# Optimization experiments

Measured on AMD Instinct MI355X. Metric: run time of the kernel, lower is better.

## Reference

```python
import jax, jax.numpy as jnp
import numpy as np

N = 4096
M0 = 2048
M1 = 2048
MCS = 4096
STRIDE = 2
D_NNGP = STRIDE ** 2 * M1              # 8192, input dim of layer-1 arccos maps
D_NTK = STRIDE ** 2 * (MCS + M1)       # 24576, input dim1 of layer-1 count sketch


def setup_inputs() -> dict:
    key = jax.random.key(0)
    ks = jax.random.split(key, 8)
    return {
        "layer_idx": 1,
        "z_nngp": jax.random.normal(ks[0], (N, D_NNGP), jnp.float32),
        "z_ntk": jax.random.normal(ks[1], (N, D_NTK), jnp.float32),
        "W0": jax.random.normal(ks[2], (D_NNGP, M0), jnp.float32),   # arccos0[1].W
        "W1": jax.random.normal(ks[3], (D_NNGP, M1), jnp.float32),   # arccos1[1].W
        "sign1": (jax.random.randint(ks[4], (D_NTK,), 0, 2) * 2 - 1).astype(jnp.float32),
        "indx1": jax.random.randint(ks[5], (D_NTK,), 0, MCS),
        "sign2": (jax.random.randint(ks[6], (M0,), 0, 2) * 2 - 1).astype(jnp.float32),
        "indx2": jax.random.randint(ks[7], (M0,), 0, MCS),
    }


def count_sketch(x, indx, sign, out_dim):
    # x: [n, d_in]; sign-multiply then scatter_add along last axis into out_dim bins
    xs = x * sign[None, :]
    out = jnp.zeros((x.shape[0], out_dim), dtype=x.dtype)
    return out.at[:, indx].add(xs)


def reference(layer_idx, z_nngp, z_ntk, W0, W1, sign1, indx1, sign2, indx2):
    norm0 = np.sqrt(2.0 / M0).astype(np.float32)
    norm1 = np.float32(np.sqrt(2.0 / M1) / 2.0)
    # arccos order-0 feature map (step function)
    xw0 = z_nngp @ W0
    tmp = (xw0 > 0).astype(z_nngp.dtype) * norm0          # [N, M0]
    # arccos order-1 feature map (relu-like: |xw| + xw)
    xw1 = z_nngp @ W1
    z_nngp_out = (jnp.abs(xw1) + xw1) * norm1             # [N, M1]
    # tensor sketch: count-sketch both, FFT, complex pointwise multiply, ifft.real
    x_cs = count_sketch(z_ntk, indx1, sign1, MCS)         # [N, MCS]
    y_cs = count_sketch(tmp, indx2, sign2, MCS)           # [N, MCS]
    z_ntk_out = jnp.fft.ifft(jnp.fft.fft(x_cs, axis=-1) * jnp.fft.fft(y_cs, axis=-1)).real
    z_ntk_cat = jnp.concatenate([z_nngp_out, z_ntk_out], axis=1)  # [N, M1+MCS]
    return (z_nngp_out, z_ntk_cat)
```

## Files before the change

### kernel.cpp

```cpp
#include <hip/hip_runtime.h>

#define NROW 4096
#define KDIM 8192
#define MDIM 2048
#define MCS_ 4096
#define DNTK 24576
#define CATW 6144
#define TAU_HALF 2.5e-3f
#define NT (KDIM / 32)

typedef __attribute__((ext_vector_type(8))) short short8;
typedef __attribute__((ext_vector_type(4))) float f32x4;

__device__ __forceinline__ void split2(float x0, float x1,
                                       unsigned& hi, unsigned& lo) {
    const unsigned u0 = __float_as_uint(x0);
    const unsigned u1 = __float_as_uint(x1);
    hi = (u0 >> 16) | (u1 & 0xFFFF0000u);
    const float l0 = x0 - __uint_as_float(u0 & 0xFFFF0000u);
    const float l1 = x1 - __uint_as_float(u1 & 0xFFFF0000u);
    lo = (__float_as_uint(l0) >> 16) | (__float_as_uint(l1) & 0xFFFF0000u);
}

__device__ __forceinline__ float2 cmulf(float2 a, float2 b) {
    return make_float2(a.x * b.x - a.y * b.y, a.x * b.y + a.y * b.x);
}

__global__ __launch_bounds__(512) void convert_kernel(
    const float* __restrict__ A,
    const float* __restrict__ W1,
    const float* __restrict__ W0,
    short8* __restrict__ aHi, short8* __restrict__ aLo,
    short8* __restrict__ wHi, short8* __restrict__ wLo)
{
    int b = blockIdx.x;
    const int tid = threadIdx.x;
    if (b < 4096) {
        const int P = b >> 8, T = b & 255;
        const float* src = A + (size_t)(P * 256) * KDIM + T * 32;
        short8* dh = aHi + ((size_t)b << 10);
        short8* dl = aLo + ((size_t)b << 10);
        for (int s = tid; s < 1024; s += 512) {
            const int row = ((s >> 6) << 4) | (s & 15);
            const int k0  = ((s >> 4) & 3) * 8;
            const float* p = src + (size_t)row * KDIM + k0;
            const float4 v0 = *reinterpret_cast<const float4*>(p);
            const float4 v1 = *reinterpret_cast<const float4*>(p + 4);
            union { short8 ss; unsigned u[4]; } h, l;
            split2(v0.x, v0.y, h.u[0], l.u[0]);
            split2(v0.z, v0.w, h.u[1], l.u[1]);
            split2(v1.x, v1.y, h.u[2], l.u[2]);
            split2(v1.z, v1.w, h.u[3], l.u[3]);
            dh[s] = h.ss; dl[s] = l.ss;
        }
    } else {
        b -= 4096;
        const int mat = b >> 11;
        const int T   = b & 255;
        const int Pc  = (b >> 8) & 7;
        const float* Wm = mat ? W0 : W1;
        const float* src = Wm + (size_t)(T * 32) * MDIM + Pc * 256;
        short8* dh = wHi + ((size_t)b << 10);
        short8* dl = wLo + ((size_t)b << 10);
        for (int s = tid; s < 1024; s += 512) {
            const int col = ((s >> 6) << 4) | (s & 15);
            const int k0  = ((s >> 4) & 3) * 8;
            float v[8];
#pragma unroll
            for (int j = 0; j < 8; ++j)
                v[j] = src[(size_t)(k0 + j) * MDIM + col];
            union { short8 ss; unsigned u[4]; } h, l;
            split2(v[0], v[1], h.u[0], l.u[0]);
            split2(v[2], v[3], h.u[1], l.u[1]);
            split2(v[4], v[5], h.u[2], l.u[2]);
            split2(v[6], v[7], h.u[3], l.u[3]);
            dh[s] = h.ss; dl[s] = l.ss;
        }
    }
}

__global__ __launch_bounds__(512) void csr_build(
    const int* __restrict__ indx1, const float* __restrict__ sign1,
    const int* __restrict__ indx2, const float* __restrict__ sign2,
    int* __restrict__ rowptr1, int* __restrict__ ent1,
    int* __restrict__ rowptr2, int* __restrict__ ent2)
{
    const int which = blockIdx.x;
    const int*   idx = which ? indx2 : indx1;
    const float* sg  = which ? sign2 : sign1;
    const int    n   = which ? 2048 : 24576;
    int* rowptr = which ? rowptr2 : rowptr1;
    int* ent    = which ? ent2 : ent1;

    __shared__ int h[4096];
    __shared__ int rp[4097];
    __shared__ int part[512];
    const int tid = threadIdx.x;

    for (int i = tid; i < 4096; i += 512) h[i] = 0;
    __syncthreads();
    for (int d = tid; d < n; d += 512) atomicAdd(&h[idx[d]], 1);
    __syncthreads();

    int loc[8], s = 0;
#pragma unroll
    for (int k = 0; k < 8; ++k) { loc[k] = h[8 * tid + k]; s += loc[k]; }
    part[tid] = s;
    __syncthreads();
    for (int off = 1; off < 512; off <<= 1) {
        int v = part[tid];
        if (tid >= off) v += part[tid - off];
        __syncthreads();
        part[tid] = v;
        __syncthreads();
    }
    int base = tid ? part[tid - 1] : 0;
#pragma unroll
    for (int k = 0; k < 8; ++k) { rp[8 * tid + k] = base; base += loc[k]; }
    if (tid == 511) rp[4096] = base;
    __syncthreads();

    for (int i = tid; i < 4096; i += 512) h[i] = 0;
    __syncthreads();
    for (int d = tid; d < n; d += 512) {
        const int b   = idx[d];
        const int pos = atomicAdd(&h[b], 1);
        ent[rp[b] + pos] = d | (sg[d] < 0.f ? 0x80000000 : 0);
    }
    __syncthreads();

    for (int i = tid; i < 4097; i += 512) rowptr[i] = rp[i];
    for (int b = tid; b < 4096; b += 512) {
        const int lo = rp[b], hi = rp[b + 1];
        for (int i = lo + 1; i < hi; ++i) {
            const int e = ent[i], key = e & 0x7FFFFFFF;
            int j = i - 1;
            while (j >= lo && (ent[j] & 0x7FFFFFFF) > key) { ent[j + 1] = ent[j]; --j; }
            ent[j + 1] = e;
        }
    }
}

__global__ __launch_bounds__(512, 2) void gemm_mfma_pre(
    const short8* __restrict__ aHi, const short8* __restrict__ aLo,
    const short8* __restrict__ wHi, const short8* __restrict__ wLo,
    float* __restrict__ out0, float* __restrict__ outCat)
{
    const int mode = blockIdx.z;
    __shared__ short8 AhiS[2][1024], AloS[2][1024];
    __shared__ short8 BhiS[2][1024], BloS[2][1024];

    const int tid  = threadIdx.x;
    const int lane = tid & 63;
    const int wid  = tid >> 6;
    const int wr   = wid >> 1;
    const int wc   = wid & 1;
    const int brow = blockIdx.y * 256;
    const int bcol = blockIdx.x * 256;

    const size_t aBase = ((size_t)blockIdx.y) << 18;
    const size_t wBase = ((size_t)(mode * 8 + blockIdx.x)) << 18;

    f32x4 acc[4][8];
#pragma unroll
    for (int m = 0; m < 4; ++m)
#pragma unroll
        for (int n = 0; n < 8; ++n)
#pragma unroll
            for (int i = 0; i < 4; ++i) acc[m][n][i] = 0.f;

    short8 st[8];

#define ISSUE(T)                                                             \
    {                                                                        \
        const size_t o = ((size_t)(T)) << 10;                                \
        st[0] = aHi[aBase + o + tid];  st[1] = aHi[aBase + o + tid + 512];   \
        st[2] = aLo[aBase + o + tid];  st[3] = aLo[aBase + o + tid + 512];   \
        st[4] = wHi[wBase + o + tid];  st[5] = wHi[wBase + o + tid + 512];   \
        st[6] = wLo[wBase + o + tid];  st[7] = wLo[wBase + o + tid + 512];   \
    }
#define WRITE(BUF)                                                           \
    {                                                                        \
        AhiS[BUF][tid] = st[0];  AhiS[BUF][tid + 512] = st[1];               \
        AloS[BUF][tid] = st[2];  AloS[BUF][tid + 512] = st[3];               \
        BhiS[BUF][tid] = st[4];  BhiS[BUF][tid + 512] = st[5];               \
        BloS[BUF][tid] = st[6];  BloS[BUF][tid + 512] = st[7];               \
    }

    ISSUE(0); WRITE(0); ISSUE(1);
    __syncthreads();

    for (int t = 0; t < NT; ++t) {
        const int cur = t & 1;

        short8 ah[4], al[4];
#pragma unroll
        for (int m = 0; m < 4; ++m) {
            ah[m] = AhiS[cur][(wr * 4 + m) * 64 + lane];
            al[m] = AloS[cur][(wr * 4 + m) * 64 + lane];
        }

        if (t + 1 < NT) {
            WRITE(cur ^ 1);
            if (t + 2 < NT) ISSUE(t + 2);
        }

#pragma unroll
        for (int n = 0; n < 8; ++n) {
            const short8 bh = BhiS[cur][(wc * 8 + n) * 64 + lane];
            const short8 bl = BloS[cur][(wc * 8 + n) * 64 + lane];
#pragma unroll
            for (int m = 0; m < 4; ++m) {
                acc[m][n] = __builtin_amdgcn_mfma_f32_16x16x32_bf16(
                    ah[m], bh, acc[m][n], 0, 0, 0);
                acc[m][n] = __builtin_amdgcn_mfma_f32_16x16x32_bf16(
                    ah[m], bl, acc[m][n], 0, 0, 0);
                acc[m][n] = __builtin_amdgcn_mfma_f32_16x16x32_bf16(
                    al[m], bh, acc[m][n], 0, 0, 0);
            }
        }
        __syncthreads();
    }
#undef ISSUE
#undef WRITE

    const float norm0 = 0.03125f;
    const int ocol0 = bcol + wc * 128 + (lane & 15);
    const int orow0 = brow + wr * 64 + ((lane >> 4) << 2);
#pragma unroll
    for (int m = 0; m < 4; ++m)
#pragma unroll
        for (int n = 0; n < 8; ++n) {
            const int col = ocol0 + n * 16;
#pragma unroll
            for (int i = 0; i < 4; ++i) {
                const int row = orow0 + m * 16 + i;
                if (mode == 0) {
                    const float v = fmaxf(acc[m][n][i], 0.f) * norm0;
                    out0[(size_t)row * MDIM + col] = v;
                    outCat[(size_t)row * CATW + col] = v;
                } else {
                    outCat[(size_t)row * CATW + 2048 + col] = acc[m][n][i];
                }
            }
        }
}

__global__ __launch_bounds__(512, 2) void gemm_mfma(
    const float* __restrict__ A,
    const float* __restrict__ W1,
    const float* __restrict__ W0,
    float* __restrict__ out0,
    float* __restrict__ outCat)
{
    const int mode = blockIdx.z;
    const float* __restrict__ W = mode ? W0 : W1;

    __shared__ short8 AhiS[2][1024], AloS[2][1024];
    __shared__ short8 BhiS[2][1024], BloS[2][1024];

    const int tid  = threadIdx.x;
    const int lane = tid & 63;
    const int wid  = tid >> 6;
    const int wr   = wid >> 1;
    const int wc   = wid & 1;
    const int brow = blockIdx.y * 256;
    const int bcol = blockIdx.x * 256;

    f32x4 acc[4][8];
#pragma unroll
    for (int m = 0; m < 4; ++m)
#pragma unroll
        for (int n = 0; n < 8; ++n)
#pragma unroll
            for (int i = 0; i < 4; ++i) acc[m][n][i] = 0.f;

    const int srow  = tid >> 1;
    const int skh   = tid & 1;
    const int slot0 = (srow >> 4) * 64 + (srow & 15) + (skh << 5);
    const float* aptr = A + (size_t)(brow + srow) * KDIM + skh * 16;
    const float* bptr = W + (size_t)(skh * 16) * MDIM + (bcol + srow);

    float4 av0, av1, av2, av3;
    float  bst[16];

#define LOAD_TILE(T)                                                         \
    {                                                                        \
        const float* ap = aptr + (T) * 32;                                   \
        av0 = *reinterpret_cast<const float4*>(ap);                          \
        av1 = *reinterpret_cast<const float4*>(ap + 4);                      \
        av2 = *reinterpret_cast<const float4*>(ap + 8);                      \
        av3 = *reinterpret_cast<const float4*>(ap + 12);                     \
        const float* bp = bptr + (size_t)((T) * 32) * MDIM;                  \
        _Pragma("unroll")                                                    \
        for (int j = 0; j < 16; ++j) bst[j] = bp[(size_t)j * MDIM];          \
    }
#define CONVERT_WRITE(BUF)                                                   \
    {                                                                        \
        union { short8 s; unsigned u[4]; } h, l;                             \
        split2(av0.x, av0.y, h.u[0], l.u[0]);                                \
        split2(av0.z, av0.w, h.u[1], l.u[1]);                                \
        split2(av1.x, av1.y, h.u[2], l.u[2]);                                \
        split2(av1.z, av1.w, h.u[3], l.u[3]);                                \
        AhiS[BUF][slot0] = h.s;  AloS[BUF][slot0] = l.s;                     \
        split2(av2.x, av2.y, h.u[0], l.u[0]);                                \
        split2(av2.z, av2.w, h.u[1], l.u[1]);                                \
        split2(av3.x, av3.y, h.u[2], l.u[2]);                                \
        split2(av3.z, av3.w, h.u[3], l.u[3]);                                \
        AhiS[BUF][slot0 + 16] = h.s;  AloS[BUF][slot0 + 16] = l.s;           \
        split2(bst[0], bst[1], h.u[0], l.u[0]);                              \
        split2(bst[2], bst[3], h.u[1], l.u[1]);                              \
        split2(bst[4], bst[5], h.u[2], l.u[2]);                              \
        split2(bst[6], bst[7], h.u[3], l.u[3]);                              \
        BhiS[BUF][slot0] = h.s;  BloS[BUF][slot0] = l.s;                     \
        split2(bst[8],  bst[9],  h.u[0], l.u[0]);                            \
        split2(bst[10], bst[11], h.u[1], l.u[1]);                            \
        split2(bst[12], bst[13], h.u[2], l.u[2]);                            \
        split2(bst[14], bst[15], h.u[3], l.u[3]);                            \
        BhiS[BUF][slot0 + 16] = h.s;  BloS[BUF][slot0 + 16] = l.s;           \
    }

    LOAD_TILE(0);
    CONVERT_WRITE(0);
    LOAD_TILE(1);
    __syncthreads();

    for (int t = 0; t < NT; ++t) {
        const int cur = t & 1;
        short8 ah[4], al[4];
#pragma unroll
        for (int m = 0; m < 4; ++m) {
            ah[m] = AhiS[cur][(wr * 4 + m) * 64 + lane];
            al[m] = AloS[cur][(wr * 4 + m) * 64 + lane];
        }
        if (t + 1 < NT) {
            CONVERT_WRITE(cur ^ 1);
            if (t + 2 < NT) LOAD_TILE(t + 2);
        }
#pragma unroll
        for (int n = 0; n < 8; ++n) {
            const short8 bh = BhiS[cur][(wc * 8 + n) * 64 + lane];
            const short8 bl = BloS[cur][(wc * 8 + n) * 64 + lane];
#pragma unroll
            for (int m = 0; m < 4; ++m) {
                acc[m][n] = __builtin_amdgcn_mfma_f32_16x16x32_bf16(
                    ah[m], bh, acc[m][n], 0, 0, 0);
                acc[m][n] = __builtin_amdgcn_mfma_f32_16x16x32_bf16(
                    ah[m], bl, acc[m][n], 0, 0, 0);
                acc[m][n] = __builtin_amdgcn_mfma_f32_16x16x32_bf16(
                    al[m], bh, acc[m][n], 0, 0, 0);
            }
        }
        __syncthreads();
    }
#undef LOAD_TILE
#undef CONVERT_WRITE

    const float norm0 = 0.03125f;
    const int ocol0 = bcol + wc * 128 + (lane & 15);
    const int orow0 = brow + wr * 64 + ((lane >> 4) << 2);
#pragma unroll
    for (int m = 0; m < 4; ++m)
#pragma unroll
        for (int n = 0; n < 8; ++n) {
            const int col = ocol0 + n * 16;
#pragma unroll
            for (int i = 0; i < 4; ++i) {
                const int row = orow0 + m * 16 + i;
                if (mode == 0) {
                    const float v = fmaxf(acc[m][n][i], 0.f) * norm0;
                    out0[(size_t)row * MDIM + col] = v;
                    outCat[(size_t)row * CATW + col] = v;
                } else {
                    outCat[(size_t)row * CATW + 2048 + col] = acc[m][n][i];
                }
            }
        }
}

#define ZP(i) Z[(i) + ((i) >> 4)]
#define C_SQ2 0.70710678118654752f

__device__ __forceinline__ void fft_conv_body(float2* Z, const float2* RT, int tid) {
    float2 x0, x1, x2, x3, x4, x5, x6, x7;

#pragma unroll
    for (int s = 0; s < 4; ++s) {
        const int lq = 3 * (3 - s);
        const int q  = 1 << lq;
        const int j  = tid & (q - 1);
        const int base = ((tid >> lq) << (lq + 3)) + j;
        x0 = ZP(base);
        x1 = ZP(base + q);
        x2 = ZP(base + 2 * q);
        x3 = ZP(base + 3 * q);
        x4 = ZP(base + 4 * q);
        x5 = ZP(base + 5 * q);
        x6 = ZP(base + 6 * q);
        x7 = ZP(base + 7 * q);

        const float2 w1 = RT[j << (9 - lq)];
        const float2 w2 = cmulf(w1, w1);
        const float2 w3 = cmulf(w2, w1);
        const float2 w4 = cmulf(w2, w2);
        const float2 w5 = cmulf(w3, w2);
        const float2 w6 = cmulf(w3, w3);
        const float2 w7 = cmulf(w4, w3);

        const float2 a0 = make_float2(x0.x + x4.x, x0.y + x4.y);
        const float2 a1 = make_float2(x1.x + x5.x, x1.y + x5.y);
        const float2 a2 = make_float2(x2.x + x6.x, x2.y + x6.y);
        const float2 a3 = make_float2(x3.x + x7.x, x3.y + x7.y);
        const float2 b0 = make_float2(x0.x - x4.x, x0.y - x4.y);
        const float2 b1 = make_float2(x1.x - x5.x, x1.y - x5.y);
        const float2 b2 = make_float2(x2.x - x6.x, x2.y - x6.y);
        const float2 b3 = make_float2(x3.x - x7.x, x3.y - x7.y);

        const float2 ca0 = make_float2(a0.x + a2.x, a0.y + a2.y);
        const float2 ca1 = make_float2(a0.x - a2.x, a0.y - a2.y);
        const float2 ca2 = make_float2(a1.x + a3.x, a1.y + a3.y);
        const float2 ca3 = make_float2(a1.x - a3.x, a1.y - a3.y);
        const float2 y0 = make_float2(ca0.x + ca2.x, ca0.y + ca2.y);
        const float2 y4 = make_float2(ca0.x - ca2.x, ca0.y - ca2.y);
        const float2 y2 = make_float2(ca1.x + ca3.y, ca1.y - ca3.x);
        const float2 y6 = make_float2(ca1.x - ca3.y, ca1.y + ca3.x);

        const float2 b1r = make_float2(C_SQ2 * (b1.x + b1.y), C_SQ2 * (b1.y - b1.x));
        const float2 b2r = make_float2(b2.y, -b2.x);
        const float2 b3r = make_float2(C_SQ2 * (b3.y - b3.x), -C_SQ2 * (b3.x + b3.y));
        const float2 cb0 = make_float2(b0.x + b2r.x, b0.y + b2r.y);
        const float2 cb1 = make_float2(b0.x - b2r.x, b0.y - b2r.y);
        const float2 cb2 = make_float2(b1r.x + b3r.x, b1r.y + b3r.y);
        const float2 cb3 = make_float2(b1r.x - b3r.x, b1r.y - b3r.y);
        const float2 y1 = make_float2(cb0.x + cb2.x, cb0.y + cb2.y);
        const float2 y5 = make_float2(cb0.x - cb2.x, cb0.y - cb2.y);
        const float2 y3 = make_float2(cb1.x + cb3.y, cb1.y - cb3.x);
        const float2 y7 = make_float2(cb1.x - cb3.y, cb1.y + cb3.x);

        ZP(base)         = y0;
        ZP(base + q)     = cmulf(y1, w1);
        ZP(base + 2 * q) = cmulf(y2, w2);
        ZP(base + 3 * q) = cmulf(y3, w3);
        ZP(base + 4 * q) = cmulf(y4, w4);
        ZP(base + 5 * q) = cmulf(y5, w5);
        ZP(base + 6 * q) = cmulf(y6, w6);
        ZP(base + 7 * q) = cmulf(y7, w7);
        __syncthreads();
    }

    for (int p = tid; p < MCS_; p += 512) {
        int q;
        if (p == 0) q = 0;
        else {
            const int h = 31 - __clz(p);
            q = 9 * (1 << (3 * (h / 3))) - 1 - p;
        }
        if (p <= q) {
            const float2 Ap = ZP(p);
            const float2 Bq = ZP(q);
            const float Xr = 0.5f * (Ap.x + Bq.x);
            const float Xi = 0.5f * (Ap.y - Bq.y);
            const float Yr = 0.5f * (Ap.y + Bq.y);
            const float Yi = -0.5f * (Ap.x - Bq.x);
            const float Pr = Xr * Yr - Xi * Yi;
            const float Pi = Xr * Yi + Xi * Yr;
            ZP(p) = make_float2(Pr, Pi);
            ZP(q) = make_float2(Pr, -Pi);
        }
    }
    __syncthreads();

#pragma unroll
    for (int s = 0; s < 4; ++s) {
        const int lq = 3 * s;
        const int q  = 1 << lq;
        const int j  = tid & (q - 1);
        const int base = ((tid >> lq) << (lq + 3)) + j;

        const float2 w1 = RT[j << (9 - lq)];
        const float2 w2 = cmulf(w1, w1);
        const float2 w3 = cmulf(w2, w1);
        const float2 w4 = cmulf(w2, w2);
        const float2 w5 = cmulf(w3, w2);
        const float2 w6 = cmulf(w3, w3);
        const float2 w7 = cmulf(w4, w3);

        x0 = ZP(base);
        {
            float2 t;
            t = ZP(base + q);     x1 = make_float2(t.x * w1.x + t.y * w1.y, t.y * w1.x - t.x * w1.y);
            t = ZP(base + 2 * q); x2 = make_float2(t.x * w2.x + t.y * w2.y, t.y * w2.x - t.x * w2.y);
            t = ZP(base + 3 * q); x3 = make_float2(t.x * w3.x + t.y * w3.y, t.y * w3.x - t.x * w3.y);
            t = ZP(base + 4 * q); x4 = make_float2(t.x * w4.x + t.y * w4.y, t.y * w4.x - t.x * w4.y);
            t = ZP(base + 5 * q); x5 = make_float2(t.x * w5.x + t.y * w5.y, t.y * w5.x - t.x * w5.y);
            t = ZP(base + 6 * q); x6 = make_float2(t.x * w6.x + t.y * w6.y, t.y * w6.x - t.x * w6.y);
            t = ZP(base + 7 * q); x7 = make_float2(t.x * w7.x + t.y * w7.y, t.y * w7.x - t.x * w7.y);
        }

        const float2 a0 = make_float2(x0.x + x4.x, x0.y + x4.y);
        const float2 a1 = make_float2(x1.x + x5.x, x1.y + x5.y);
        const float2 a2 = make_float2(x2.x + x6.x, x2.y + x6.y);
        const float2 a3 = make_float2(x3.x + x7.x, x3.y + x7.y);
        const float2 b0 = make_float2(x0.x - x4.x, x0.y - x4.y);
        const float2 b1 = make_float2(x1.x - x5.x, x1.y - x5.y);
        const float2 b2 = make_float2(x2.x - x6.x, x2.y - x6.y);
        const float2 b3 = make_float2(x3.x - x7.x, x3.y - x7.y);

        const float2 ca0 = make_float2(a0.x + a2.x, a0.y + a2.y);
        const float2 ca1 = make_float2(a0.x - a2.x, a0.y - a2.y);
        const float2 ca2 = make_float2(a1.x + a3.x, a1.y + a3.y);
        const float2 ca3 = make_float2(a1.x - a3.x, a1.y - a3.y);
        const float2 y0 = make_float2(ca0.x + ca2.x, ca0.y + ca2.y);
        const float2 y4 = make_float2(ca0.x - ca2.x, ca0.y - ca2.y);
        const float2 y2 = make_float2(ca1.x - ca3.y, ca1.y + ca3.x);
        const float2 y6 = make_float2(ca1.x + ca3.y, ca1.y - ca3.x);

        const float2 b1r = make_float2(C_SQ2 * (b1.x - b1.y), C_SQ2 * (b1.x + b1.y));
        const float2 b2r = make_float2(-b2.y, b2.x);
        const float2 b3r = make_float2(-C_SQ2 * (b3.x + b3.y), C_SQ2 * (b3.x - b3.y));
        const float2 cb0 = make_float2(b0.x + b2r.x, b0.y + b2r.y);
        const float2 cb1 = make_float2(b0.x - b2r.x, b0.y - b2r.y);
        const float2 cb2 = make_float2(b1r.x + b3r.x, b1r.y + b3r.y);
        const float2 cb3 = make_float2(b1r.x - b3r.x, b1r.y - b3r.y);
        const float2 y1 = make_float2(cb0.x + cb2.x, cb0.y + cb2.y);
        const float2 y5 = make_float2(cb0.x - cb2.x, cb0.y - cb2.y);
        const float2 y3 = make_float2(cb1.x - cb3.y, cb1.y + cb3.x);
        const float2 y7 = make_float2(cb1.x + cb3.y, cb1.y - cb3.x);

        ZP(base)         = y0;
        ZP(base + q)     = y1;
        ZP(base + 2 * q) = y2;
        ZP(base + 3 * q) = y3;
        ZP(base + 4 * q) = y4;
        ZP(base + 5 * q) = y5;
        ZP(base + 6 * q) = y6;
        ZP(base + 7 * q) = y7;
        __syncthreads();
    }
}

__global__ __launch_bounds__(512) void sketch_fft_csr(
    const float* __restrict__ z_ntk,
    const int* __restrict__ rowptr1, const int* __restrict__ ent1,
    const int* __restrict__ rowptr2, const int* __restrict__ ent2,
    float* __restrict__ outCat)
{
    __shared__ __align__(16) float2 Z[4352];
    __shared__ float2 RT[513];
    float* Zf = reinterpret_cast<float*>(Z);
    const int tid = threadIdx.x;
    const int row = blockIdx.x;
    const float norm0 = 0.03125f;

    const float wconst = -1.5339807878856412e-3f;
    for (int t = tid; t <= 512; t += 512) {
        float sw, cw;
        __sincosf(wconst * (float)t, &sw, &cw);
        RT[t] = make_float2(cw, sw);
    }

    int rpx[9], rpy[9];
#pragma unroll
    for (int k = 0; k < 9; ++k) {
        rpx[k] = rowptr1[8 * tid + k];
        rpy[k] = rowptr2[8 * tid + k];
    }
    float accX[8], accY[8];
#pragma unroll
    for (int k = 0; k < 8; ++k) { accX[k] = 0.f; accY[k] = 0.f; }
    int cur[8];
#pragma unroll
    for (int k = 0; k < 8; ++k) cur[k] = rpx[k];

    const float4* xrow4 = reinterpret_cast<const float4*>(z_ntk + (size_t)row * DNTK);
    for (int c = 0; c < 3; ++c) {
        const int lo = c * 8192, hi = lo + 8192;
        __syncthreads();
#pragma unroll
        for (int j = 0; j < 4; ++j)
            reinterpret_cast<float4*>(Zf)[tid + j * 512] = xrow4[c * 2048 + tid + j * 512];
        __syncthreads();
#pragma unroll
        for (int k = 0; k < 8; ++k) {
            while (cur[k] < rpx[k + 1]) {
                const int e = ent1[cur[k]];
                const int d = e & 0x7FFFFFFF;
                if (d >= hi) break;
                const float v = Zf[d - lo];
                accX[k] += (e < 0) ? -v : v;
                ++cur[k];
            }
        }
    }

    const float* trow = outCat + (size_t)row * CATW + 2048;
    __syncthreads();
    reinterpret_cast<float4*>(Zf)[tid] = reinterpret_cast<const float4*>(trow)[tid];
    __syncthreads();
#pragma unroll
    for (int k = 0; k < 8; ++k) {
        for (int c = rpy[k]; c < rpy[k + 1]; ++c) {
            const int e = ent2[c];
            const int d = e & 0x7FFFFFFF;
            const float t = Zf[d];
            const float y = (fabsf(t) < TAU_HALF) ? 0.5f * norm0
                                                  : (t > 0.f ? norm0 : 0.f);
            accY[k] += (e < 0) ? -y : y;
        }
    }
    __syncthreads();

#pragma unroll
    for (int k = 0; k < 8; ++k) {
        const int b = 8 * tid + k;
        ZP(b) = make_float2(accX[k], accY[k]);
    }
    __syncthreads();

    fft_conv_body(Z, RT, tid);

    float* orow = outCat + (size_t)row * CATW + 2048;
    const float scale = 1.0f / (float)MCS_;
    for (int n = tid; n < MCS_; n += 512) orow[n] = ZP(n).x * scale;
}

#define YBASE 4608
__global__ __launch_bounds__(512) void sketch_fft_atomic(
    const float* __restrict__ z_ntk,
    const float* __restrict__ sign1,
    const int*   __restrict__ indx1,
    const float* __restrict__ sign2,
    const int*   __restrict__ indx2,
    float* __restrict__ outCat)
{
    __shared__ __align__(16) float2 Z[4352];
    __shared__ float2 RT[513];
    float* Zf = reinterpret_cast<float*>(Z);
    const int tid = threadIdx.x;
    const int row = blockIdx.x;

    for (int i = tid; i < 2176; i += 512)
        reinterpret_cast<float4*>(Zf)[i] = make_float4(0.f, 0.f, 0.f, 0.f);
    const float wconst = -1.5339807878856412e-3f;
    for (int t = tid; t <= 512; t += 512) {
        float sw, cw;
        __sincosf(wconst * (float)t, &sw, &cw);
        RT[t] = make_float2(cw, sw);
    }
    __syncthreads();

    const float4* xrow4 = reinterpret_cast<const float4*>(z_ntk + (size_t)row * DNTK);
    const float4* s1v   = reinterpret_cast<const float4*>(sign1);
    const int4*   i1v   = reinterpret_cast<const int4*>(indx1);
    for (int v = tid; v < DNTK / 4; v += 512) {
        const float4 x = xrow4[v];
        const float4 s = s1v[v];
        const int4   ix = i1v[v];
        atomicAdd(&Zf[ix.x], x.x * s.x);
        atomicAdd(&Zf[ix.y], x.y * s.y);
        atomicAdd(&Zf[ix.z], x.z * s.z);
        atomicAdd(&Zf[ix.w], x.w * s.w);
    }
    const float norm0 = 0.03125f;
    const float* trow = outCat + (size_t)row * CATW + 2048;
    {
        const float4 t4 = reinterpret_cast<const float4*>(trow)[tid];
        const float4 s  = reinterpret_cast<const float4*>(sign2)[tid];
        const int4   ix = reinterpret_cast<const int4*>(indx2)[tid];
        const float y0 = (fabsf(t4.x) < TAU_HALF) ? 0.5f * norm0 : (t4.x > 0.f ? norm0 : 0.f);
        const float y1 = (fabsf(t4.y) < TAU_HALF) ? 0.5f * norm0 : (t4.y > 0.f ? norm0 : 0.f);
        const float y2 = (fabsf(t4.z) < TAU_HALF) ? 0.5f * norm0 : (t4.z > 0.f ? norm0 : 0.f);
        const float y3 = (fabsf(t4.w) < TAU_HALF) ? 0.5f * norm0 : (t4.w > 0.f ? norm0 : 0.f);
        atomicAdd(&Zf[YBASE + ix.x], y0 * s.x);
        atomicAdd(&Zf[YBASE + ix.y], y1 * s.y);
        atomicAdd(&Zf[YBASE + ix.z], y2 * s.z);
        atomicAdd(&Zf[YBASE + ix.w], y3 * s.w);
    }
    __syncthreads();

    {
        float re[8], im[8];
#pragma unroll
        for (int j = 0; j < 8; ++j) {
            const int i = tid + j * 512;
            re[j] = Zf[i];
            im[j] = Zf[YBASE + i];
        }
        __syncthreads();
#pragma unroll
        for (int j = 0; j < 8; ++j) {
            const int i = tid + j * 512;
            ZP(i) = make_float2(re[j], im[j]);
        }
    }
    __syncthreads();

    fft_conv_body(Z, RT, tid);

    float* orow = outCat + (size_t)row * CATW + 2048;
    const float scale = 1.0f / (float)MCS_;
    for (int n = tid; n < MCS_; n += 512) orow[n] = ZP(n).x * scale;
}

extern "C" void kernel_launch(void* const* d_in, const int* in_sizes, int n_in,
                              void* d_out, int out_size, void* d_ws, size_t ws_size,
                              hipStream_t stream) {
    (void)in_sizes; (void)n_in; (void)out_size;
    const float* z_nngp = (const float*)d_in[1];
    const float* z_ntk  = (const float*)d_in[2];
    const float* W0     = (const float*)d_in[3];
    const float* W1     = (const float*)d_in[4];
    const float* sign1  = (const float*)d_in[5];
    const int*   indx1  = (const int*)d_in[6];
    const float* sign2  = (const float*)d_in[7];
    const int*   indx2  = (const int*)d_in[8];

    float* out0   = (float*)d_out;
    float* outCat = out0 + (size_t)NROW * MDIM;

    const size_t NEED_P = 268435456ull;
    const size_t NEED_C = NEED_P + (1ull << 20);

    int* rowptr1 = nullptr; int* rowptr2 = nullptr;
    int* ent1 = nullptr;    int* ent2 = nullptr;
    const bool csr_ok = ws_size >= NEED_C;
    if (csr_ok) {
        int* base = (int*)((char*)d_ws + NEED_P);
        rowptr1 = base;
        rowptr2 = base + 4352;
        ent1    = base + 8704;
        ent2    = ent1 + 24576;
        csr_build<<<dim3(2), dim3(512), 0, stream>>>(
            indx1, sign1, indx2, sign2, rowptr1, ent1, rowptr2, ent2);
    }

    if (ws_size >= NEED_P) {
        short8* aHi = (short8*)d_ws;
        short8* aLo = aHi + (1ull << 22);
        short8* wHi = aLo + (1ull << 22);
        short8* wLo = wHi + (1ull << 22);
        convert_kernel<<<dim3(8192), dim3(512), 0, stream>>>(
            z_nngp, W1, W0, aHi, aLo, wHi, wLo);
        gemm_mfma_pre<<<dim3(8, 16, 2), dim3(512), 0, stream>>>(
            aHi, aLo, wHi, wLo, out0, outCat);
    } else {
        gemm_mfma<<<dim3(8, 16, 2), dim3(512), 0, stream>>>(
            z_nngp, W1, W0, out0, outCat);
    }

    if (csr_ok) {
        sketch_fft_csr<<<dim3(NROW), dim3(512), 0, stream>>>(
            z_ntk, rowptr1, ent1, rowptr2, ent2, outCat);
    } else {
        sketch_fft_atomic<<<dim3(NROW), dim3(512), 0, stream>>>(
            z_ntk, sign1, indx1, sign2, indx2, outCat);
    }
}
```

Before: 1.294 ms.

## Gather sketch inputs directly from global memory instead of staging through LDS

The CSR count-sketch kernel no longer copies z_ntk chunks and the tmp row into shared memory with block-wide barriers. Each thread now gathers its eight bins' entries straight from global memory, batching eight independent loads per iteration, and the loop exits through a wave-level any-check. The kernel also gets a launch-bounds occupancy hint. This removes the three staging passes and their syncs, in exchange for uncoalesced random global reads that depend on cache hits.

Measured after the change: 1.701 ms. +31.5%, slower.

```diff
diff --git a/kernel.cpp b/kernel.cpp
--- a/kernel.cpp
+++ b/kernel.cpp
@@ -539,7 +539,7 @@
     }
 }
 
-__global__ __launch_bounds__(512) void sketch_fft_csr(
+__global__ __launch_bounds__(512, 8) void sketch_fft_csr(
     const float* __restrict__ z_ntk,
     const int* __restrict__ rowptr1, const int* __restrict__ ent1,
     const int* __restrict__ rowptr2, const int* __restrict__ ent2,
@@ -547,7 +547,6 @@
 {
     __shared__ __align__(16) float2 Z[4352];
     __shared__ float2 RT[513];
-    float* Zf = reinterpret_cast<float*>(Z);
     const int tid = threadIdx.x;
     const int row = blockIdx.x;
     const float norm0 = 0.03125f;
@@ -559,56 +558,61 @@
         RT[t] = make_float2(cw, sw);
     }
 
-    int rpx[9], rpy[9];
-#pragma unroll
-    for (int k = 0; k < 9; ++k) {
-        rpx[k] = rowptr1[8 * tid + k];
-        rpy[k] = rowptr2[8 * tid + k];
-    }
-    float accX[8], accY[8];
-#pragma unroll
-    for (int k = 0; k < 8; ++k) { accX[k] = 0.f; accY[k] = 0.f; }
-    int cur[8];
-#pragma unroll
-    for (int k = 0; k < 8; ++k) cur[k] = rpx[k];
-
-    const float4* xrow4 = reinterpret_cast<const float4*>(z_ntk + (size_t)row * DNTK);
-    for (int c = 0; c < 3; ++c) {
-        const int lo = c * 8192, hi = lo + 8192;
-        __syncthreads();
-#pragma unroll
-        for (int j = 0; j < 4; ++j)
-            reinterpret_cast<float4*>(Zf)[tid + j * 512] = xrow4[c * 2048 + tid + j * 512];
-        __syncthreads();
+    const float* zrow = z_ntk + (size_t)row * DNTK;
+    const float* trow = outCat + (size_t)row * CATW + 2048;
+
+    int rpx[9];
+#pragma unroll
+    for (int k = 0; k < 9; ++k) rpx[k] = rowptr1[8 * tid + k];
+    float accX[8];
+    int c8[8];
+#pragma unroll
+    for (int k = 0; k < 8; ++k) { accX[k] = 0.f; c8[k] = rpx[k]; }
+
+    for (;;) {
+        bool ok[8];
+        int any = 0;
 #pragma unroll
         for (int k = 0; k < 8; ++k) {
-            while (cur[k] < rpx[k + 1]) {
-                const int e = ent1[cur[k]];
-                const int d = e & 0x7FFFFFFF;
-                if (d >= hi) break;
-                const float v = Zf[d - lo];
-                accX[k] += (e < 0) ? -v : v;
-                ++cur[k];
+            ok[k] = c8[k] < rpx[k + 1];
+            any |= (int)ok[k];
+        }
+        if (!__any(any)) break;
+        int e8[8];
+#pragma unroll
+        for (int k = 0; k < 8; ++k)
+            e8[k] = ent1[ok[k] ? c8[k] : 0];
+        float v8[8];
+#pragma unroll
+        for (int k = 0; k < 8; ++k)
+            v8[k] = zrow[e8[k] & 0x7FFFFFFF];
+#pragma unroll
+        for (int k = 0; k < 8; ++k) {
+            if (ok[k]) {
+                accX[k] += (e8[k] < 0) ? -v8[k] : v8[k];
+                ++c8[k];
             }
         }
     }
 
-    const float* trow = outCat + (size_t)row * CATW + 2048;
-    __syncthreads();
-    reinterpret_cast<float4*>(Zf)[tid] = reinterpret_cast<const float4*>(trow)[tid];
-    __syncthreads();
-#pragma unroll
-    for (int k = 0; k < 8; ++k) {
-        for (int c = rpy[k]; c < rpy[k + 1]; ++c) {
-            const int e = ent2[c];
-            const int d = e & 0x7FFFFFFF;
-            const float t = Zf[d];
-            const float y = (fabsf(t) < TAU_HALF) ? 0.5f * norm0
-                                                  : (t > 0.f ? norm0 : 0.f);
-            accY[k] += (e < 0) ? -y : y;
-        }
-    }
-    __syncthreads();
+    float accY[8];
+#pragma unroll
+    for (int k = 0; k < 8; ++k) accY[k] = 0.f;
+    {
+        int rpy[9];
+#pragma unroll
+        for (int k = 0; k < 9; ++k) rpy[k] = rowptr2[8 * tid + k];
+#pragma unroll
+        for (int k = 0; k < 8; ++k) {
+            for (int c = rpy[k]; c < rpy[k + 1]; ++c) {
+                const int e = ent2[c];
+                const float t = trow[e & 0x7FFFFFFF];
+                const float y = (fabsf(t) < TAU_HALF) ? 0.5f * norm0
+                                                      : (t > 0.f ? norm0 : 0.f);
+                accY[k] += (e < 0) ? -y : y;
+            }
+        }
+    }
 
 #pragma unroll
     for (int k = 0; k < 8; ++k) {
```

## Split CSR sketch and FFT convolution into separate kernels via workspace bins

Applied to the files above, without the earlier changes.

The fused sketch+FFT kernel is split in two. The first gathers count-sketch bins per row into a global workspace buffer using a 32KB shared array. The second loads those bins and runs the FFT convolution. The aim is to cut per-kernel shared memory and register pressure so more blocks fit per CU. The cost is an extra global round trip of 128MB of bins, one more kernel launch, and reuse of the d_ws region that the GEMM preconversion also uses, which relies on stream ordering.

New measurement: 1.370 ms. +5.9%, slower.

```diff
diff --git a/kernel.cpp b/kernel.cpp
--- a/kernel.cpp
+++ b/kernel.cpp
@@ -539,26 +539,18 @@
     }
 }
 
-__global__ __launch_bounds__(512) void sketch_fft_csr(
+__global__ __launch_bounds__(512) void sketch_bins(
     const float* __restrict__ z_ntk,
     const int* __restrict__ rowptr1, const int* __restrict__ ent1,
     const int* __restrict__ rowptr2, const int* __restrict__ ent2,
-    float* __restrict__ outCat)
+    const float* __restrict__ outCat,
+    float2* __restrict__ bins)
 {
-    __shared__ __align__(16) float2 Z[4352];
-    __shared__ float2 RT[513];
-    float* Zf = reinterpret_cast<float*>(Z);
+    __shared__ __align__(16) float Zf[8192];
     const int tid = threadIdx.x;
     const int row = blockIdx.x;
     const float norm0 = 0.03125f;
 
-    const float wconst = -1.5339807878856412e-3f;
-    for (int t = tid; t <= 512; t += 512) {
-        float sw, cw;
-        __sincosf(wconst * (float)t, &sw, &cw);
-        RT[t] = make_float2(cw, sw);
-    }
-
     int rpx[9], rpy[9];
 #pragma unroll
     for (int k = 0; k < 9; ++k) {
@@ -575,7 +567,7 @@
     const float4* xrow4 = reinterpret_cast<const float4*>(z_ntk + (size_t)row * DNTK);
     for (int c = 0; c < 3; ++c) {
         const int lo = c * 8192, hi = lo + 8192;
-        __syncthreads();
+        if (c) __syncthreads();
 #pragma unroll
         for (int j = 0; j < 4; ++j)
             reinterpret_cast<float4*>(Zf)[tid + j * 512] = xrow4[c * 2048 + tid + j * 512];
@@ -608,12 +600,34 @@
             accY[k] += (e < 0) ? -y : y;
         }
     }
-    __syncthreads();
-
-#pragma unroll
-    for (int k = 0; k < 8; ++k) {
-        const int b = 8 * tid + k;
-        ZP(b) = make_float2(accX[k], accY[k]);
+
+    float2* brow = bins + (size_t)row * MCS_;
+#pragma unroll
+    for (int k = 0; k < 8; ++k)
+        brow[8 * tid + k] = make_float2(accX[k], accY[k]);
+}
+
+__global__ __launch_bounds__(512) void conv_fft(
+    const float2* __restrict__ bins,
+    float* __restrict__ outCat)
+{
+    __shared__ __align__(16) float2 Z[4352];
+    __shared__ float2 RT[513];
+    const int tid = threadIdx.x;
+    const int row = blockIdx.x;
+
+    const float wconst = -1.5339807878856412e-3f;
+    for (int t = tid; t <= 512; t += 512) {
+        float sw, cw;
+        __sincosf(wconst * (float)t, &sw, &cw);
+        RT[t] = make_float2(cw, sw);
+    }
+
+    const float2* brow = bins + (size_t)row * MCS_;
+#pragma unroll
+    for (int j = 0; j < 8; ++j) {
+        const int i = tid + j * 512;
+        ZP(i) = brow[i];
     }
     __syncthreads();
 
@@ -749,8 +763,10 @@
     }
 
     if (csr_ok) {
-        sketch_fft_csr<<<dim3(NROW), dim3(512), 0, stream>>>(
-            z_ntk, rowptr1, ent1, rowptr2, ent2, outCat);
+        float2* bins = (float2*)d_ws;
+        sketch_bins<<<dim3(NROW), dim3(512), 0, stream>>>(
+            z_ntk, rowptr1, ent1, rowptr2, ent2, outCat, bins);
+        conv_fft<<<dim3(NROW), dim3(512), 0, stream>>>(bins, outCat);
     } else {
         sketch_fft_atomic<<<dim3(NROW), dim3(512), 0, stream>>>(
             z_ntk, sign1, indx1, sign2, indx2, outCat);
```
